# Kernel tuning notes

Hardware: AMD Instinct MI355X
Metric: run time of the kernel (lower is better)

The kernel has to match this reference:

```python
import jax, jax.numpy as jnp
import numpy as np

S, N, A = 64, 4096, 32
HID, DM, NH, DK = 256, 128, 4, 32
EPS = 1e-5
SCALE = float(np.sqrt(DK))


def setup_inputs() -> dict:
    key = jax.random.key(0)
    ks = jax.random.split(key, 20)
    w = lambda i, sh: jax.random.normal(ks[i], sh, jnp.float32) * 0.02
    z = lambda n: jnp.zeros((n,), jnp.float32)
    return {
        "agent_states": jax.random.normal(ks[0], (N, S), jnp.float32),
        "sw1": w(1, (N * S, HID)), "sb1": z(HID),
        "sw2": w(2, (HID, HID)), "sb2": z(HID),
        "sow": w(3, (HID, 64)), "sob": z(64),
        "tw": w(4, (S + 64, DM)), "tb": z(DM),
        "wq": w(5, (DM, DM)), "bq": z(DM),
        "wk": w(6, (DM, DM)), "bk": z(DM),
        "wv": w(7, (DM, DM)), "bv": z(DM),
        "wo": w(8, (DM, DM)), "bo": z(DM),
        "ln_g": jnp.ones((DM,), jnp.float32), "ln_b": z(DM),
        "taw1": w(9, (DM, 64)), "tab1": z(64),
        "taw2": w(10, (64, 32)), "tab2": z(32),
        "ow1": w(11, (S + DM + 32, 256)), "ob1": z(256),
        "ow2": w(12, (256, DM)), "ob2": z(DM),
        "aw": w(13, (DM, A)), "ab": z(A),
        "vw": w(14, (DM, 1)), "vb": z(1),
        "cw": w(15, (S, 64)), "cb": z(64),
        "cdw": w(16, (64, 32)), "cdb": z(32),
    }


def reference(agent_states, sw1, sb1, sw2, sb2, sow, sob, tw, tb,
              wq, bq, wk, bk, wv, bv, wo, bo, ln_g, ln_b,
              taw1, tab1, taw2, tab2, ow1, ob1, ow2, ob2,
              aw, ab, vw, vb, cw, cb, cdw, cdb):
    n = agent_states.shape[0]
    # strategic level: flatten all agent states -> global objective [64]
    gs = agent_states.reshape(-1)
    strat = jax.nn.relu(jax.nn.relu(gs @ sw1 + sb1) @ sw2 + sb2)
    gobj = strat @ sow + sob
    # tactical encode (batched over agents instead of Python loop)
    tact_in = jnp.concatenate(
        [agent_states, jnp.broadcast_to(gobj, (n, gobj.shape[0]))], axis=-1)
    tact = jax.nn.relu(tact_in @ tw + tb)[None]  # [1, n, DM]
    # multi-head attention across agents
    q = (tact @ wq + bq).reshape(1, n, NH, DK).transpose(0, 2, 1, 3)
    k = (tact @ wk + bk).reshape(1, n, NH, DK).transpose(0, 2, 1, 3)
    v = (tact @ wv + bv).reshape(1, n, NH, DK).transpose(0, 2, 1, 3)
    scores = jnp.einsum('bhqd,bhkd->bhqk', q, k) / SCALE
    attn = jax.nn.softmax(scores, axis=-1)  # [1, NH, n, n]
    ctx = jnp.einsum('bhqk,bhkd->bhqd', attn, v).transpose(0, 2, 1, 3).reshape(1, n, DM)
    res = ctx @ wo + bo + tact
    mu = res.mean(-1, keepdims=True)
    var = res.var(-1, keepdims=True)  # biased, like torch LayerNorm
    coord = ((res - mu) / jnp.sqrt(var + EPS) * ln_g + ln_b)[0]  # [n, DM]
    # task allocation (softmax over 32 tasks)
    task = jax.nn.softmax(jax.nn.relu(coord @ taw1 + tab1) @ taw2 + tab2, axis=-1)
    # operational level -> actions / values
    op_in = jnp.concatenate([agent_states, coord, task], axis=-1)
    opf = jax.nn.relu(jax.nn.relu(op_in @ ow1 + ob1) @ ow2 + ob2)
    actions = opf @ aw + ab
    values = opf @ vw + vb
    # communication messages (two stacked linears, no activation in source)
    messages = (agent_states @ cw + cb) @ cdw + cdb
    return actions, values, messages, task, attn, gobj
```

## Files before the change

kernel.cpp:

```cpp
#include <hip/hip_runtime.h>

typedef __attribute__((ext_vector_type(8))) short s8v;
typedef __attribute__((ext_vector_type(4))) short s4v;
typedef __attribute__((ext_vector_type(4))) float f4v;

#define MFMA16(a, b, c) __builtin_amdgcn_mfma_f32_16x16x32_bf16((a), (b), (c), 0, 0, 0)

#define LDS_BARRIER do {                                        \
    __builtin_amdgcn_sched_barrier(0);                          \
    asm volatile("s_waitcnt lgkmcnt(0)" ::: "memory");          \
    __builtin_amdgcn_s_barrier();                               \
    __builtin_amdgcn_sched_barrier(0);                          \
} while (0)

#define NAG   4096
#define SDIM  64
#define DMOD  128
#define NHD   4
#define DKD   32
#define HIDD  256
static constexpr float INV_SCALE = 0.17677669529663687f;
static constexpr float EPSV = 1e-5f;

#define OFF_ACT   0
#define OFF_VAL   131072
#define OFF_MSG   135168
#define OFF_TASK  266240
#define OFF_ATTN  397312
#define OFF_GOBJ  67506176

static constexpr size_t WS_P1   = 0;
static constexpr size_t WS_P1B  = 524288;
static constexpr size_t WS_P2   = 540672;
static constexpr size_t WS_TACT = 558080;
static constexpr size_t WS_Q    = 2655232;
static constexpr size_t WS_K    = 3703808;
static constexpr size_t WS_VT   = 4752384;
static constexpr size_t WS_CTX  = 5800960;
static constexpr size_t WS_OPIN = 7898112;
static constexpr size_t WS_H    = 9733120;
static constexpr size_t WS_OPF  = 11830272;
static constexpr size_t WS_OW1T = 12878848;
static constexpr size_t WS_OW2T = 12993536;

typedef unsigned short u16;
typedef unsigned int   u32;

static __device__ __forceinline__ u16 f2bf(float f) {
    union { float f; u32 u; } x; x.f = f;
    u32 r = x.u + 0x7FFFu + ((x.u >> 16) & 1u);
    return (u16)(r >> 16);
}
static __device__ __forceinline__ float bf2f(u16 b) {
    union { u32 u; float f; } x; x.u = ((u32)b) << 16;
    return x.f;
}

__global__ __launch_bounds__(256) void k1_sw1(const float* __restrict__ gs,
                                              const float* __restrict__ sw1,
                                              float* __restrict__ p1,
                                              const float* __restrict__ ow1,
                                              const float* __restrict__ ow2,
                                              u16* __restrict__ w1t,
                                              u16* __restrict__ w2t) {
    int tid = threadIdx.x;
    int b = blockIdx.x;
    if (b >= 512) {
        int bb = b - 512;
        if (bb < 224) {
            w1t[tid * 224 + bb] = f2bf(ow1[bb * 256 + tid]);
        } else if (tid < 128) {
            int k0 = (bb - 224) * 8;
#pragma unroll
            for (int kk = 0; kk < 8; ++kk) {
                int k = k0 + kk;
                w2t[tid * 256 + k] = f2bf(ow2[k * 128 + tid]);
            }
        }
        return;
    }
    __shared__ float gsl[512];
    __shared__ float red[4][256];
    gsl[tid]       = gs[b * 512 + tid];
    gsl[tid + 256] = gs[b * 512 + 256 + tid];
    __syncthreads();
    int t = tid & 63;
    int rg = tid >> 6;
    const f4v* w4 = (const f4v*)sw1;
    f4v acc = {0.f, 0.f, 0.f, 0.f};
    size_t rb = (size_t)b * 512;
#pragma unroll 4
    for (int r = rg; r < 512; r += 4) {
        float g = gsl[r];
        f4v w = __builtin_nontemporal_load(&w4[(rb + r) * 64 + t]);
        acc[0] += g * w[0]; acc[1] += g * w[1]; acc[2] += g * w[2]; acc[3] += g * w[3];
    }
    red[rg][4 * t + 0] = acc[0]; red[rg][4 * t + 1] = acc[1];
    red[rg][4 * t + 2] = acc[2]; red[rg][4 * t + 3] = acc[3];
    __syncthreads();
    float s = red[0][tid] + red[1][tid] + red[2][tid] + red[3][tid];
    p1[b * 256 + tid] = s;
}

__global__ void k1b_red(const float* __restrict__ p1, float* __restrict__ p1b) {
    int j = threadIdx.x;
    int b0 = blockIdx.x * 32;
    float s = 0.f;
#pragma unroll
    for (int b = 0; b < 32; ++b) s += p1[(b0 + b) * 256 + j];
    p1b[blockIdx.x * 256 + j] = s;
}

__global__ void k2b_strat(const float* __restrict__ p1b, const float* __restrict__ sb1,
                          const float* __restrict__ sw2, float* __restrict__ p2) {
    __shared__ float h1[256];
    int j = threadIdx.x;
    float s = 0.f;
#pragma unroll
    for (int b = 0; b < 16; ++b) s += p1b[b * 256 + j];
    h1[j] = fmaxf(s + sb1[j], 0.f);
    __syncthreads();
    int i0 = blockIdx.x * 16;
    float acc = 0.f;
#pragma unroll
    for (int i = 0; i < 16; ++i) acc += h1[i0 + i] * sw2[(i0 + i) * 256 + j];
    p2[blockIdx.x * 256 + j] = acc;
}

__global__ __launch_bounds__(256) void k3_tact_qkv(
    const float* __restrict__ p2, const float* __restrict__ sb2,
    const float* __restrict__ sow, const float* __restrict__ sob,
    const float* __restrict__ as, const float* __restrict__ tw, const float* __restrict__ tb,
    const float* __restrict__ wq, const float* __restrict__ bq,
    const float* __restrict__ wk, const float* __restrict__ bk,
    const float* __restrict__ wv, const float* __restrict__ bv,
    float* __restrict__ out_gobj, float* __restrict__ tactws,
    u16* __restrict__ qws, u16* __restrict__ kws, u16* __restrict__ vtws) {
    __shared__ float strat[256];
    __shared__ float gobj[64];
    __shared__ float asl[8][64];
    __shared__ float tl[8][128];
    int tid = threadIdx.x;
    int a0 = blockIdx.x * 8;
    {
        float s = 0.f;
#pragma unroll
        for (int b = 0; b < 16; ++b) s += p2[b * 256 + tid];
        strat[tid] = fmaxf(s + sb2[tid], 0.f);
    }
#pragma unroll
    for (int r = 0; r < 2; ++r) {
        int idx = tid + r * 256;
        asl[idx >> 6][idx & 63] = as[a0 * 64 + idx];
    }
    __syncthreads();
    if (tid < 64) {
        float g = sob[tid];
        for (int i = 0; i < 256; ++i) g += strat[i] * sow[i * 64 + tid];
        gobj[tid] = g;
        if (blockIdx.x == 0) out_gobj[tid] = g;
    }
    __syncthreads();
    int ah = tid >> 7, j = tid & 127;
    float gacc = 0.f;
    for (int i = 0; i < 64; ++i) gacc += gobj[i] * tw[(64 + i) * 128 + j];
    float acc[4];
    float base = tb[j] + gacc;
#pragma unroll
    for (int a = 0; a < 4; ++a) acc[a] = base;
    for (int i = 0; i < 64; ++i) {
        float w = tw[i * 128 + j];
#pragma unroll
        for (int a = 0; a < 4; ++a) acc[a] += asl[ah * 4 + a][i] * w;
    }
#pragma unroll
    for (int a = 0; a < 4; ++a) {
        float t = fmaxf(acc[a], 0.f);
        tl[ah * 4 + a][j] = t;
        tactws[(size_t)(a0 + ah * 4 + a) * 128 + j] = t;
    }
    __syncthreads();
    int h = j >> 5, d = j & 31;
#pragma unroll
    for (int a = 0; a < 4; ++a) acc[a] = 0.f;
    for (int i = 0; i < 128; ++i) {
        float w = wq[i * 128 + j];
#pragma unroll
        for (int a = 0; a < 4; ++a) acc[a] += tl[ah * 4 + a][i] * w;
    }
#pragma unroll
    for (int a = 0; a < 4; ++a)
        qws[h * 131072 + (a0 + ah * 4 + a) * 32 + d] = f2bf((acc[a] + bq[j]) * INV_SCALE);
#pragma unroll
    for (int a = 0; a < 4; ++a) acc[a] = 0.f;
    for (int i = 0; i < 128; ++i) {
        float w = wk[i * 128 + j];
#pragma unroll
        for (int a = 0; a < 4; ++a) acc[a] += tl[ah * 4 + a][i] * w;
    }
#pragma unroll
    for (int a = 0; a < 4; ++a)
        kws[h * 131072 + (a0 + ah * 4 + a) * 32 + d] = f2bf(acc[a] + bk[j]);
#pragma unroll
    for (int a = 0; a < 4; ++a) acc[a] = 0.f;
    for (int i = 0; i < 128; ++i) {
        float w = wv[i * 128 + j];
#pragma unroll
        for (int a = 0; a < 4; ++a) acc[a] += tl[ah * 4 + a][i] * w;
    }
    union { u16 u[4]; s4v v; } pk;
#pragma unroll
    for (int a = 0; a < 4; ++a) pk.u[a] = f2bf(acc[a] + bv[j]);
    *(s4v*)(vtws + h * 131072 + d * 4096 + a0 + ah * 4) = pk.v;
}

__global__ __launch_bounds__(512) void k4_attn(
    const u16* __restrict__ qws, const u16* __restrict__ kws, const u16* __restrict__ vtws,
    float* __restrict__ attn, float* __restrict__ ctxws) {
    int tid = threadIdx.x;
    int wid = tid >> 6;
    int l = tid & 63;
    int g = l >> 4;
    int ln = l & 15;
    int h = blockIdx.x >> 8;
    int qt = (blockIdx.x & 255) * 16;
    const u16* qh = qws + h * 131072;
    const u16* kh = kws + h * 131072;
    const u16* vh = vtws + h * 131072;
    int j0 = wid * 512;

    s8v aq = *(const s8v*)(qh + (qt + ln) * 32 + 8 * g);
    f4v zero = {0.f, 0.f, 0.f, 0.f};

    __shared__ __align__(16) union SmemU {
        float red[8][16];
        float sT[2][16][260];
        float pctx[8][16][32];
    } sm;

    f4v lacc = zero;
    for (int jc = 0; jc < 16; ++jc) {
        int jb = j0 + jc * 32;
        s8v b0 = *(const s8v*)(kh + (jb + ln) * 32 + 8 * g);
        s8v b1 = *(const s8v*)(kh + (jb + 16 + ln) * 32 + 8 * g);
        f4v S0 = MFMA16(aq, b0, zero);
        f4v S1 = MFMA16(aq, b1, zero);
#pragma unroll
        for (int r = 0; r < 4; ++r)
            lacc[r] += __expf(S0[r]) + __expf(S1[r]);
    }
#pragma unroll
    for (int m = 1; m <= 8; m <<= 1) {
        lacc[0] += __shfl_xor(lacc[0], m);
        lacc[1] += __shfl_xor(lacc[1], m);
        lacc[2] += __shfl_xor(lacc[2], m);
        lacc[3] += __shfl_xor(lacc[3], m);
    }
    if (ln == 0) {
#pragma unroll
        for (int r = 0; r < 4; ++r) sm.red[wid][4 * g + r] = lacc[r];
    }
    __syncthreads();
    float linvq = 1.f / (sm.red[0][ln] + sm.red[1][ln] + sm.red[2][ln] + sm.red[3][ln] +
                         sm.red[4][ln] + sm.red[5][ln] + sm.red[6][ln] + sm.red[7][ln]);
    __syncthreads();

    float* attnh = attn + (size_t)h * 4096 * 4096;
    f4v accA = zero, accB = zero;
    int co = wid * 32;
    auto COMPUTE = [&](int c, int p) {
        int jb = c * 256 + co;
        s8v b0 = *(const s8v*)(kh + (jb + ln) * 32 + 8 * g);
        s8v b1 = *(const s8v*)(kh + (jb + 16 + ln) * 32 + 8 * g);
        f4v S0 = MFMA16(b0, aq, zero);
        f4v S1 = MFMA16(b1, aq, zero);
        f4v o0, o1;
#pragma unroll
        for (int r = 0; r < 4; ++r) {
            o0[r] = __expf(S0[r]) * linvq;
            o1[r] = __expf(S1[r]) * linvq;
        }
        *(f4v*)&sm.sT[p][ln][co + 4 * g] = o0;
        *(f4v*)&sm.sT[p][ln][co + 16 + 4 * g] = o1;
    };
    auto PVSTORE = [&](int c, int p) {
        int jb = c * 256 + co;
        f4v t0 = *(const f4v*)&sm.sT[p][ln][co + 8 * g];
        f4v t1 = *(const f4v*)&sm.sT[p][ln][co + 8 * g + 4];
        union { u16 u[8]; s8v v; } bp;
#pragma unroll
        for (int i = 0; i < 4; ++i) { bp.u[i] = f2bf(t0[i]); bp.u[4 + i] = f2bf(t1[i]); }
        s8v va = *(const s8v*)(vh + ln * 4096 + jb + 8 * g);
        s8v vb = *(const s8v*)(vh + (16 + ln) * 4096 + jb + 8 * g);
        accA = MFMA16(va, bp.v, accA);
        accB = MFMA16(vb, bp.v, accB);
#pragma unroll
        for (int r2 = 0; r2 < 2; ++r2) {
            int row = 2 * wid + r2;
            f4v t = *(const f4v*)&sm.sT[p][row][4 * l];
            *(f4v*)(attnh + (size_t)(qt + row) * 4096 + c * 256 + 4 * l) = t;
        }
    };
    COMPUTE(0, 0);
    LDS_BARRIER;
    for (int c = 1; c < 16; ++c) {
        PVSTORE(c - 1, (c - 1) & 1);
        COMPUTE(c, c & 1);
        LDS_BARRIER;
    }
    PVSTORE(15, 1);
    __syncthreads();

#pragma unroll
    for (int r = 0; r < 4; ++r) {
        sm.pctx[wid][ln][4 * g + r] = accA[r];
        sm.pctx[wid][ln][16 + 4 * g + r] = accB[r];
    }
    __syncthreads();
    {
        int q = tid >> 5;
        int d = tid & 31;
        float s = sm.pctx[0][q][d] + sm.pctx[1][q][d] + sm.pctx[2][q][d] + sm.pctx[3][q][d] +
                  sm.pctx[4][q][d] + sm.pctx[5][q][d] + sm.pctx[6][q][d] + sm.pctx[7][q][d];
        ctxws[(size_t)(qt + q) * 128 + h * 32 + d] = s;
    }
}

__global__ __launch_bounds__(512) void k5_post(
    const float* __restrict__ ctxws, const float* __restrict__ tactws,
    const float* __restrict__ wo, const float* __restrict__ bo,
    const float* __restrict__ lng, const float* __restrict__ lnb,
    const float* __restrict__ taw1, const float* __restrict__ tab1,
    const float* __restrict__ taw2, const float* __restrict__ tab2,
    const float* __restrict__ as, float* __restrict__ dout, u16* __restrict__ opin) {
    __shared__ float wos[128 * 128];
    __shared__ float tw1s[128 * 64];
    __shared__ float tw2s[64 * 32];
    __shared__ float cx[8][128];
    __shared__ float coords[8][128];
    __shared__ float t1v[8][64];
    int tid = threadIdx.x;
    for (int i = tid; i < 128 * 128; i += 512) wos[i] = wo[i];
    for (int i = tid; i < 128 * 64; i += 512) tw1s[i] = taw1[i];
    for (int i = tid; i < 64 * 32; i += 512) tw2s[i] = taw2[i];
    __syncthreads();
    int w = tid >> 6, l = tid & 63;
    for (int it = 0; it < 2; ++it) {
        int n = blockIdx.x * 16 + w * 2 + it;
        float c0 = ctxws[(size_t)n * 128 + l], c1 = ctxws[(size_t)n * 128 + 64 + l];
        float t0 = tactws[(size_t)n * 128 + l], t1 = tactws[(size_t)n * 128 + 64 + l];
        float av = as[n * 64 + l];
        cx[w][l] = c0; cx[w][64 + l] = c1;
        float r0 = bo[l] + t0, r1 = bo[64 + l] + t1;
        for (int k = 0; k < 128; ++k) {
            float cv = cx[w][k];
            r0 += cv * wos[k * 128 + l];
            r1 += cv * wos[k * 128 + 64 + l];
        }
        float s = r0 + r1;
#pragma unroll
        for (int m = 1; m <= 32; m <<= 1) s += __shfl_xor(s, m);
        float mu = s * (1.f / 128.f);
        float d0 = r0 - mu, d1 = r1 - mu;
        float vs = d0 * d0 + d1 * d1;
#pragma unroll
        for (int m = 1; m <= 32; m <<= 1) vs += __shfl_xor(vs, m);
        float rstd = 1.f / sqrtf(vs * (1.f / 128.f) + EPSV);
        float co0 = d0 * rstd * lng[l] + lnb[l];
        float co1 = d1 * rstd * lng[64 + l] + lnb[64 + l];
        coords[w][l] = co0; coords[w][64 + l] = co1;
        opin[(size_t)n * 224 + l] = f2bf(av);
        opin[(size_t)n * 224 + 64 + l] = f2bf(co0);
        opin[(size_t)n * 224 + 128 + l] = f2bf(co1);
        float a1 = tab1[l];
        for (int i = 0; i < 128; ++i) a1 += coords[w][i] * tw1s[i * 64 + l];
        t1v[w][l] = fmaxf(a1, 0.f);
        if (l < 32) {
            float a2 = tab2[l];
            for (int i = 0; i < 64; ++i) a2 += t1v[w][i] * tw2s[i * 32 + l];
            float mx = a2;
#pragma unroll
            for (int m = 1; m <= 16; m <<= 1) mx = fmaxf(mx, __shfl_xor(mx, m));
            float e = __expf(a2 - mx);
            float se = e;
#pragma unroll
            for (int m = 1; m <= 16; m <<= 1) se += __shfl_xor(se, m);
            float tk = e / se;
            dout[OFF_TASK + n * 32 + l] = tk;
            opin[(size_t)n * 224 + 192 + l] = f2bf(tk);
        }
    }
}

__global__ __launch_bounds__(256) void k6a(const u16* __restrict__ opin, const u16* __restrict__ w1t,
                                           const float* __restrict__ ob1, u16* __restrict__ Hws) {
    int tid = threadIdx.x;
    int w = tid >> 6, l = tid & 63, g = l >> 4, ln = l & 15;
    int bm = blockIdx.x & 63, bn = blockIdx.x >> 6;
    int m0 = bm * 64 + w * 16, n0 = bn * 64;
    f4v acc[4];
    f4v zero = {0.f, 0.f, 0.f, 0.f};
#pragma unroll
    for (int nt = 0; nt < 4; ++nt) acc[nt] = zero;
    for (int kt = 0; kt < 7; ++kt) {
        s8v A = *(const s8v*)(opin + (size_t)(m0 + ln) * 224 + kt * 32 + 8 * g);
#pragma unroll
        for (int nt = 0; nt < 4; ++nt) {
            s8v B = *(const s8v*)(w1t + (size_t)(n0 + nt * 16 + ln) * 224 + kt * 32 + 8 * g);
            acc[nt] = MFMA16(A, B, acc[nt]);
        }
    }
#pragma unroll
    for (int nt = 0; nt < 4; ++nt) {
        int col = n0 + nt * 16 + ln;
        float bias = ob1[col];
#pragma unroll
        for (int r = 0; r < 4; ++r) {
            int row = m0 + 4 * g + r;
            Hws[(size_t)row * 256 + col] = f2bf(fmaxf(acc[nt][r] + bias, 0.f));
        }
    }
}

__global__ __launch_bounds__(256) void k6b(const u16* __restrict__ Hws, const u16* __restrict__ w2t,
                                           const float* __restrict__ ob2, u16* __restrict__ opfws) {
    int tid = threadIdx.x;
    int w = tid >> 6, l = tid & 63, g = l >> 4, ln = l & 15;
    int bm = blockIdx.x & 63, bn = blockIdx.x >> 6;
    int m0 = bm * 64 + w * 16, n0 = bn * 64;
    f4v acc[4];
    f4v zero = {0.f, 0.f, 0.f, 0.f};
#pragma unroll
    for (int nt = 0; nt < 4; ++nt) acc[nt] = zero;
    for (int kt = 0; kt < 8; ++kt) {
        s8v A = *(const s8v*)(Hws + (size_t)(m0 + ln) * 256 + kt * 32 + 8 * g);
#pragma unroll
        for (int nt = 0; nt < 4; ++nt) {
            s8v B = *(const s8v*)(w2t + (size_t)(n0 + nt * 16 + ln) * 256 + kt * 32 + 8 * g);
            acc[nt] = MFMA16(A, B, acc[nt]);
        }
    }
#pragma unroll
    for (int nt = 0; nt < 4; ++nt) {
        int col = n0 + nt * 16 + ln;
        float bias = ob2[col];
#pragma unroll
        for (int r = 0; r < 4; ++r) {
            int row = m0 + 4 * g + r;
            opfws[(size_t)row * 128 + col] = f2bf(fmaxf(acc[nt][r] + bias, 0.f));
        }
    }
}

__global__ __launch_bounds__(256) void k6c(const u16* __restrict__ opf, const float* __restrict__ as,
                                           const float* __restrict__ aw, const float* __restrict__ ab,
                                           const float* __restrict__ vw, const float* __restrict__ vb,
                                           const float* __restrict__ cw, const float* __restrict__ cb,
                                           const float* __restrict__ cdw, const float* __restrict__ cdb,
                                           float* __restrict__ dout) {
    __shared__ float opfs[4][128];
    __shared__ float asl[4][64];
    __shared__ float m1s[4][64];
    int tid = threadIdx.x;
    int w = tid >> 6, l = tid & 63;
    int n = blockIdx.x * 4 + w;
    {
        u32 u = *(const u32*)(opf + (size_t)n * 128 + 2 * l);
        opfs[w][2 * l] = bf2f((u16)(u & 0xffff));
        opfs[w][2 * l + 1] = bf2f((u16)(u >> 16));
        asl[w][l] = as[n * 64 + l];
    }
    __syncthreads();
    if (l < 32) {
        float a = ab[l];
        for (int k = 0; k < 128; ++k) a += opfs[w][k] * aw[k * 32 + l];
        dout[OFF_ACT + n * 32 + l] = a;
    }
    {
        float p = opfs[w][l] * vw[l] + opfs[w][64 + l] * vw[64 + l];
#pragma unroll
        for (int m = 1; m <= 32; m <<= 1) p += __shfl_xor(p, m);
        if (l == 0) dout[OFF_VAL + n] = p + vb[0];
    }
    {
        float a = cb[l];
        for (int k = 0; k < 64; ++k) a += asl[w][k] * cw[k * 64 + l];
        m1s[w][l] = a;
    }
    __syncthreads();
    if (l < 32) {
        float a = cdb[l];
        for (int k = 0; k < 64; ++k) a += m1s[w][k] * cdw[k * 32 + l];
        dout[OFF_MSG + n * 32 + l] = a;
    }
}

extern "C" void kernel_launch(void* const* d_in, const int* in_sizes, int n_in,
                              void* d_out, int out_size, void* d_ws, size_t ws_size,
                              hipStream_t stream) {
    const float* as  = (const float*)d_in[0];
    const float* sw1 = (const float*)d_in[1];
    const float* sb1 = (const float*)d_in[2];
    const float* sw2 = (const float*)d_in[3];
    const float* sb2 = (const float*)d_in[4];
    const float* sow = (const float*)d_in[5];
    const float* sob = (const float*)d_in[6];
    const float* tw  = (const float*)d_in[7];
    const float* tb  = (const float*)d_in[8];
    const float* wq  = (const float*)d_in[9];
    const float* bq  = (const float*)d_in[10];
    const float* wk  = (const float*)d_in[11];
    const float* bk  = (const float*)d_in[12];
    const float* wv  = (const float*)d_in[13];
    const float* bv  = (const float*)d_in[14];
    const float* wo  = (const float*)d_in[15];
    const float* bo  = (const float*)d_in[16];
    const float* lng = (const float*)d_in[17];
    const float* lnb = (const float*)d_in[18];
    const float* taw1 = (const float*)d_in[19];
    const float* tab1 = (const float*)d_in[20];
    const float* taw2 = (const float*)d_in[21];
    const float* tab2 = (const float*)d_in[22];
    const float* ow1 = (const float*)d_in[23];
    const float* ob1 = (const float*)d_in[24];
    const float* ow2 = (const float*)d_in[25];
    const float* ob2 = (const float*)d_in[26];
    const float* aw  = (const float*)d_in[27];
    const float* ab  = (const float*)d_in[28];
    const float* vw  = (const float*)d_in[29];
    const float* vb  = (const float*)d_in[30];
    const float* cw  = (const float*)d_in[31];
    const float* cb  = (const float*)d_in[32];
    const float* cdw = (const float*)d_in[33];
    const float* cdb = (const float*)d_in[34];

    float* dout = (float*)d_out;
    char* ws = (char*)d_ws;
    float* p1    = (float*)(ws + WS_P1);
    float* p1b   = (float*)(ws + WS_P1B);
    float* p2    = (float*)(ws + WS_P2);
    float* tactw = (float*)(ws + WS_TACT);
    u16*   qws   = (u16*)(ws + WS_Q);
    u16*   kws   = (u16*)(ws + WS_K);
    u16*   vtws  = (u16*)(ws + WS_VT);
    float* ctxws = (float*)(ws + WS_CTX);
    u16*   opin  = (u16*)(ws + WS_OPIN);
    u16*   Hws   = (u16*)(ws + WS_H);
    u16*   opfws = (u16*)(ws + WS_OPF);
    u16*   w1t   = (u16*)(ws + WS_OW1T);
    u16*   w2t   = (u16*)(ws + WS_OW2T);

    hipLaunchKernelGGL(k1_sw1, dim3(768), dim3(256), 0, stream, as, sw1, p1, ow1, ow2, w1t, w2t);
    hipLaunchKernelGGL(k1b_red, dim3(16), dim3(256), 0, stream, p1, p1b);
    hipLaunchKernelGGL(k2b_strat, dim3(16), dim3(256), 0, stream, p1b, sb1, sw2, p2);
    hipLaunchKernelGGL(k3_tact_qkv, dim3(512), dim3(256), 0, stream,
                       p2, sb2, sow, sob, as, tw, tb, wq, bq, wk, bk, wv, bv,
                       dout + OFF_GOBJ, tactw, qws, kws, vtws);
    hipLaunchKernelGGL(k4_attn, dim3(1024), dim3(512), 0, stream,
                       qws, kws, vtws, dout + OFF_ATTN, ctxws);
    hipLaunchKernelGGL(k5_post, dim3(256), dim3(512), 0, stream,
                       ctxws, tactw, wo, bo, lng, lnb, taw1, tab1, taw2, tab2, as, dout, opin);
    hipLaunchKernelGGL(k6a, dim3(256), dim3(256), 0, stream, opin, w1t, ob1, Hws);
    hipLaunchKernelGGL(k6b, dim3(128), dim3(256), 0, stream, Hws, w2t, ob2, opfws);
    hipLaunchKernelGGL(k6c, dim3(1024), dim3(256), 0, stream,
                       opfws, as, aw, ab, vw, vb, cw, cb, cdw, cdb, dout);
}
```

Measured before the change: 190.9 us.

## Process two query tiles per attention block, overlapping second tile's row-sum pass

The attention kernel now handles 32 queries per block as two 16-query tiles, halving the grid. The softmax-denominator pass for the second tile is interleaved into the main score/PV/store loop of the first tile, so its exp and MFMA work can hide behind the attention-matrix writes. The cost is more registers, a longer serial body per block, and fewer blocks (512) to fill the GPU.

```diff
diff --git a/kernel.cpp b/kernel.cpp
--- a/kernel.cpp
+++ b/kernel.cpp
@@ -222,68 +222,69 @@
     int l = tid & 63;
     int g = l >> 4;
     int ln = l & 15;
-    int h = blockIdx.x >> 8;
-    int qt = (blockIdx.x & 255) * 16;
+    int h = blockIdx.x >> 7;
+    int qt = (blockIdx.x & 127) * 32;
     const u16* qh = qws + h * 131072;
     const u16* kh = kws + h * 131072;
     const u16* vh = vtws + h * 131072;
     int j0 = wid * 512;
-
-    s8v aq = *(const s8v*)(qh + (qt + ln) * 32 + 8 * g);
+    int co = wid * 32;
+
+    s8v aq0 = *(const s8v*)(qh + (qt + ln) * 32 + 8 * g);
+    s8v aq1 = *(const s8v*)(qh + (qt + 16 + ln) * 32 + 8 * g);
     f4v zero = {0.f, 0.f, 0.f, 0.f};
 
+    __shared__ float red2[2][8][16];
     __shared__ __align__(16) union SmemU {
-        float red[8][16];
         float sT[2][16][260];
         float pctx[8][16][32];
     } sm;
 
-    f4v lacc = zero;
-    for (int jc = 0; jc < 16; ++jc) {
+    float* attnh = attn + (size_t)h * 4096 * 4096;
+
+    auto ALEAN = [&](int jc, s8v aqv, f4v& lac) {
         int jb = j0 + jc * 32;
         s8v b0 = *(const s8v*)(kh + (jb + ln) * 32 + 8 * g);
         s8v b1 = *(const s8v*)(kh + (jb + 16 + ln) * 32 + 8 * g);
-        f4v S0 = MFMA16(aq, b0, zero);
-        f4v S1 = MFMA16(aq, b1, zero);
+        f4v S0 = MFMA16(aqv, b0, zero);
+        f4v S1 = MFMA16(aqv, b1, zero);
 #pragma unroll
         for (int r = 0; r < 4; ++r)
-            lacc[r] += __expf(S0[r]) + __expf(S1[r]);
-    }
-#pragma unroll
-    for (int m = 1; m <= 8; m <<= 1) {
-        lacc[0] += __shfl_xor(lacc[0], m);
-        lacc[1] += __shfl_xor(lacc[1], m);
-        lacc[2] += __shfl_xor(lacc[2], m);
-        lacc[3] += __shfl_xor(lacc[3], m);
-    }
-    if (ln == 0) {
-#pragma unroll
-        for (int r = 0; r < 4; ++r) sm.red[wid][4 * g + r] = lacc[r];
-    }
-    __syncthreads();
-    float linvq = 1.f / (sm.red[0][ln] + sm.red[1][ln] + sm.red[2][ln] + sm.red[3][ln] +
-                         sm.red[4][ln] + sm.red[5][ln] + sm.red[6][ln] + sm.red[7][ln]);
-    __syncthreads();
-
-    float* attnh = attn + (size_t)h * 4096 * 4096;
-    f4v accA = zero, accB = zero;
-    int co = wid * 32;
-    auto COMPUTE = [&](int c, int p) {
+            lac[r] += __expf(S0[r]) + __expf(S1[r]);
+    };
+    auto REDSUM = [&](f4v lac, int which) {
+#pragma unroll
+        for (int m = 1; m <= 8; m <<= 1) {
+            lac[0] += __shfl_xor(lac[0], m);
+            lac[1] += __shfl_xor(lac[1], m);
+            lac[2] += __shfl_xor(lac[2], m);
+            lac[3] += __shfl_xor(lac[3], m);
+        }
+        if (ln == 0) {
+#pragma unroll
+            for (int r = 0; r < 4; ++r) red2[which][wid][4 * g + r] = lac[r];
+        }
+    };
+    auto LINV = [&](int which) {
+        return 1.f / (red2[which][0][ln] + red2[which][1][ln] + red2[which][2][ln] + red2[which][3][ln] +
+                      red2[which][4][ln] + red2[which][5][ln] + red2[which][6][ln] + red2[which][7][ln]);
+    };
+    auto COMPUTE = [&](int c, int p, s8v aqv, float linv) {
         int jb = c * 256 + co;
         s8v b0 = *(const s8v*)(kh + (jb + ln) * 32 + 8 * g);
         s8v b1 = *(const s8v*)(kh + (jb + 16 + ln) * 32 + 8 * g);
-        f4v S0 = MFMA16(b0, aq, zero);
-        f4v S1 = MFMA16(b1, aq, zero);
+        f4v S0 = MFMA16(b0, aqv, zero);
+        f4v S1 = MFMA16(b1, aqv, zero);
         f4v o0, o1;
 #pragma unroll
         for (int r = 0; r < 4; ++r) {
-            o0[r] = __expf(S0[r]) * linvq;
-            o1[r] = __expf(S1[r]) * linvq;
+            o0[r] = __expf(S0[r]) * linv;
+            o1[r] = __expf(S1[r]) * linv;
         }
         *(f4v*)&sm.sT[p][ln][co + 4 * g] = o0;
         *(f4v*)&sm.sT[p][ln][co + 16 + 4 * g] = o1;
     };
-    auto PVSTORE = [&](int c, int p) {
+    auto PVSTORE = [&](int c, int p, int qbase, f4v& aA, f4v& aB) {
         int jb = c * 256 + co;
         f4v t0 = *(const f4v*)&sm.sT[p][ln][co + 8 * g];
         f4v t1 = *(const f4v*)&sm.sT[p][ln][co + 8 * g + 4];
@@ -292,37 +293,74 @@
         for (int i = 0; i < 4; ++i) { bp.u[i] = f2bf(t0[i]); bp.u[4 + i] = f2bf(t1[i]); }
         s8v va = *(const s8v*)(vh + ln * 4096 + jb + 8 * g);
         s8v vb = *(const s8v*)(vh + (16 + ln) * 4096 + jb + 8 * g);
-        accA = MFMA16(va, bp.v, accA);
-        accB = MFMA16(vb, bp.v, accB);
+        aA = MFMA16(va, bp.v, aA);
+        aB = MFMA16(vb, bp.v, aB);
 #pragma unroll
         for (int r2 = 0; r2 < 2; ++r2) {
             int row = 2 * wid + r2;
             f4v t = *(const f4v*)&sm.sT[p][row][4 * l];
-            *(f4v*)(attnh + (size_t)(qt + row) * 4096 + c * 256 + 4 * l) = t;
+            *(f4v*)(attnh + (size_t)(qbase + row) * 4096 + c * 256 + 4 * l) = t;
         }
     };
-    COMPUTE(0, 0);
+
+    {
+        f4v l0 = zero;
+        for (int jc = 0; jc < 16; ++jc) ALEAN(jc, aq0, l0);
+        REDSUM(l0, 0);
+    }
+    __syncthreads();
+    float linv0 = LINV(0);
+
+    f4v acc0A = zero, acc0B = zero, l1 = zero;
+    COMPUTE(0, 0, aq0, linv0);
+    ALEAN(0, aq1, l1);
     LDS_BARRIER;
     for (int c = 1; c < 16; ++c) {
-        PVSTORE(c - 1, (c - 1) & 1);
-        COMPUTE(c, c & 1);
+        PVSTORE(c - 1, (c - 1) & 1, qt, acc0A, acc0B);
+        COMPUTE(c, c & 1, aq0, linv0);
+        ALEAN(c, aq1, l1);
         LDS_BARRIER;
     }
-    PVSTORE(15, 1);
+    PVSTORE(15, 1, qt, acc0A, acc0B);
+    REDSUM(l1, 1);
+    __syncthreads();
+    float linv1 = LINV(1);
+
+    f4v acc1A = zero, acc1B = zero;
+    COMPUTE(0, 0, aq1, linv1);
+    LDS_BARRIER;
+    for (int c = 1; c < 16; ++c) {
+        PVSTORE(c - 1, (c - 1) & 1, qt + 16, acc1A, acc1B);
+        COMPUTE(c, c & 1, aq1, linv1);
+        LDS_BARRIER;
+    }
+    PVSTORE(15, 1, qt + 16, acc1A, acc1B);
     __syncthreads();
 
 #pragma unroll
     for (int r = 0; r < 4; ++r) {
-        sm.pctx[wid][ln][4 * g + r] = accA[r];
-        sm.pctx[wid][ln][16 + 4 * g + r] = accB[r];
+        sm.pctx[wid][ln][4 * g + r] = acc0A[r];
+        sm.pctx[wid][ln][16 + 4 * g + r] = acc0B[r];
     }
     __syncthreads();
     {
-        int q = tid >> 5;
-        int d = tid & 31;
+        int q = tid >> 5, d = tid & 31;
         float s = sm.pctx[0][q][d] + sm.pctx[1][q][d] + sm.pctx[2][q][d] + sm.pctx[3][q][d] +
                   sm.pctx[4][q][d] + sm.pctx[5][q][d] + sm.pctx[6][q][d] + sm.pctx[7][q][d];
         ctxws[(size_t)(qt + q) * 128 + h * 32 + d] = s;
+    }
+    __syncthreads();
+#pragma unroll
+    for (int r = 0; r < 4; ++r) {
+        sm.pctx[wid][ln][4 * g + r] = acc1A[r];
+        sm.pctx[wid][ln][16 + 4 * g + r] = acc1B[r];
+    }
+    __syncthreads();
+    {
+        int q = tid >> 5, d = tid & 31;
+        float s = sm.pctx[0][q][d] + sm.pctx[1][q][d] + sm.pctx[2][q][d] + sm.pctx[3][q][d] +
+                  sm.pctx[4][q][d] + sm.pctx[5][q][d] + sm.pctx[6][q][d] + sm.pctx[7][q][d];
+        ctxws[(size_t)(qt + 16 + q) * 128 + h * 32 + d] = s;
     }
 }
 
@@ -556,7 +594,7 @@
     hipLaunchKernelGGL(k3_tact_qkv, dim3(512), dim3(256), 0, stream,
                        p2, sb2, sow, sob, as, tw, tb, wq, bq, wk, bk, wv, bv,
                        dout + OFF_GOBJ, tactw, qws, kws, vtws);
-    hipLaunchKernelGGL(k4_attn, dim3(1024), dim3(512), 0, stream,
+    hipLaunchKernelGGL(k4_attn, dim3(512), dim3(512), 0, stream,
                        qws, kws, vtws, dout + OFF_ATTN, ctxws);
     hipLaunchKernelGGL(k5_post, dim3(256), dim3(512), 0, stream,
                        ctxws, tactw, wo, bo, lng, lnb, taw1, tab1, taw2, tab2, as, dout, opin);
```

New measurement: 199.6 us. +4.5%, slower.
